# Kernel tuning notes

Hardware: AMD Instinct MI355X
Metric: run time of the kernel (lower is better)

## Reference

```python
import jax, jax.numpy as jnp
import numpy as np

TEMP = 10.0
D_IN, D_HID, D_OUT = 256, 512, 256
B, M = 4, 4096


def _mlp(x, W1, b1, W2, b2):
    # two-layer MLP, ReLU hidden, linear output ('cnt' = continuous)
    h = jax.nn.relu(jnp.einsum('bmd,dh->bmh', x, W1) + b1)
    return jnp.einsum('bmh,ho->bmo', h, W2) + b2


def setup_inputs() -> dict:
    key = jax.random.key(0)
    ks = jax.random.split(key, 9)
    s1 = 1.0 / np.sqrt(D_IN)
    s2 = 1.0 / np.sqrt(D_HID)
    return {
        'x': jax.random.normal(ks[0], (B, M, D_IN), dtype=jnp.float32),
        'Wq1': jax.random.normal(ks[1], (D_IN, D_HID), dtype=jnp.float32) * s1,
        'bq1': jnp.zeros((D_HID,), dtype=jnp.float32),
        'Wq2': jax.random.normal(ks[2], (D_HID, D_OUT), dtype=jnp.float32) * s2,
        'bq2': jnp.zeros((D_OUT,), dtype=jnp.float32),
        'Wk1': jax.random.normal(ks[3], (D_IN, D_HID), dtype=jnp.float32) * s1,
        'bk1': jnp.zeros((D_HID,), dtype=jnp.float32),
        'Wk2': jax.random.normal(ks[4], (D_HID, D_OUT), dtype=jnp.float32) * s2,
        'bk2': jnp.zeros((D_OUT,), dtype=jnp.float32),
    }


def reference(x, Wq1, bq1, Wq2, bq2, Wk1, bk1, Wk2, bk2):
    queries = _mlp(x, Wq1, bq1, Wq2, bq2)   # [B, M, D_OUT]
    keys = _mlp(x, Wk1, bk1, Wk2, bk2)      # [B, M, D_OUT]
    qkt = jnp.einsum('bnd,bmd->bnm', queries, keys)  # [B, M, M]
    row_max = jnp.max(qkt, axis=-1, keepdims=True)   # row-max normalization (not sqrt(d))
    dist = jax.nn.softmax(TEMP * qkt / row_max, axis=-1)
    return dist
```

## Files before the change

### kernel.cpp

```cpp
#include <hip/hip_runtime.h>
#include <hip/hip_bf16.h>

typedef unsigned short u16;
typedef unsigned int u32;
typedef _Float16 f16;
typedef __attribute__((ext_vector_type(4))) float f32x4;
typedef __attribute__((ext_vector_type(8))) short s16x8;
typedef __attribute__((ext_vector_type(8))) _Float16 f16x8;

__device__ __forceinline__ u16 f2bf(float f) {
    union { float f; u32 u; } v; v.f = f;
    u32 r = v.u + 0x7FFFu + ((v.u >> 16) & 1u);
    return (u16)(r >> 16);
}
__device__ __forceinline__ float bf2f(u16 h) {
    union { u32 u; float f; } v; v.u = ((u32)h) << 16;
    return v.f;
}

__device__ __forceinline__ void gll16(const void* g, void* l) {
    __builtin_amdgcn_global_load_lds(
        (const __attribute__((address_space(1))) void*)g,
        (__attribute__((address_space(3))) void*)l, 16, 0, 0);
}


__global__ __launch_bounds__(256) void split_x_kernel(
    const float* __restrict__ x, u16* __restrict__ hi, u16* __restrict__ lo) {
    int i = blockIdx.x * 256 + threadIdx.x;
    float4 v = ((const float4*)x)[i];
    u16 h0 = f2bf(v.x), h1 = f2bf(v.y), h2 = f2bf(v.z), h3 = f2bf(v.w);
    ushort4 h, l;
    h.x = h0; h.y = h1; h.z = h2; h.w = h3;
    l.x = f2bf(v.x - bf2f(h0)); l.y = f2bf(v.y - bf2f(h1));
    l.z = f2bf(v.z - bf2f(h2)); l.w = f2bf(v.w - bf2f(h3));
    ((ushort4*)hi)[i] = h; ((ushort4*)lo)[i] = l;
}

__global__ __launch_bounds__(256) void split_wT_kernel(
    const float* __restrict__ Wq1, const float* __restrict__ Wk1,
    const float* __restrict__ Wq2, const float* __restrict__ Wk2,
    u16* __restrict__ w1hi, u16* __restrict__ w1lo,
    u16* __restrict__ w2hi, u16* __restrict__ w2lo) {
    int y = blockIdx.y;
    const float* src = (y == 0) ? Wq1 : (y == 1) ? Wk1 : (y == 2) ? Wq2 : Wk2;
    int R = (y < 2) ? 256 : 512;
    int C = (y < 2) ? 512 : 256;
    u16* dh = ((y < 2) ? w1hi : w2hi) + (y & 1) * 131072;
    u16* dl = ((y < 2) ? w1lo : w2lo) + (y & 1) * 131072;
    int i = blockIdx.x * 256 + threadIdx.x;
    int c = i / R, r = i - c * R;
    float v = src[(size_t)r * C + c];
    u16 h = f2bf(v);
    dh[i] = h; dl[i] = f2bf(v - bf2f(h));
}

__global__ void pack_bias(const float* __restrict__ bq1, const float* __restrict__ bk1,
                          const float* __restrict__ bq2, const float* __restrict__ bk2,
                          float* __restrict__ b1, float* __restrict__ b2) {
    int t = threadIdx.x;
    b1[t] = bq1[t]; b1[512 + t] = bk1[t];
    if (t < 256) { b2[t] = bq2[t]; b2[256 + t] = bk2[t]; }
}

#define BM 128
#define BN 128
#define BK 64

template<int SPLIT_OUT, int RELU, int SPLITB, int F16S>
__global__ __launch_bounds__(256, 2)
void gemm_bt(const u16* __restrict__ Ahi, const u16* __restrict__ Alo,
             const u16* __restrict__ Bhi, const u16* __restrict__ Blo,
             const float* __restrict__ bias, long biasBatch,
             void* __restrict__ Cout, u16* __restrict__ Chi, u16* __restrict__ Clo,
             int M, int N, int K,
             long aBatch, long bBatch, long cBatch) {
    __shared__ u16 lds[(3 + SPLITB) * BM * BK];
    const int tid = threadIdx.x;
    const int wave = tid >> 6, lane = tid & 63;

    u32 gx = gridDim.x, gy = gridDim.y, gz = gridDim.z;
    u32 flat = (blockIdx.z * gy + blockIdx.y) * gx + blockIdx.x;
    u32 nwg = gx * gy * gz;
    u32 bx, by, bz;
    if ((nwg & 7u) == 0u) {
        u32 cpx = nwg >> 3;
        u32 nf = (flat & 7u) * cpx + (flat >> 3);
        bx = nf % gx; u32 t = nf / gx; by = t % gy; bz = t / gy;
    } else {
        bx = blockIdx.x; by = blockIdx.y; bz = blockIdx.z;
    }

    const long m0 = (long)by * BM, n0 = (long)bx * BN;

    const u16* pAhi = Ahi + (size_t)bz * aBatch;
    const u16* pAlo = Alo + (size_t)bz * aBatch;
    const u16* pBhi = Bhi + (size_t)bz * bBatch;
    const u16* pBlo = Blo + (size_t)bz * bBatch;

    int srow[4], scol[4];
#pragma unroll
    for (int i = 0; i < 4; i++) {
        int lin = wave * 4096 + i * 1024 + lane * 16;
        srow[i] = lin >> 7;
        scol[i] = (lin & 127) >> 1;
    }

    const int wr = wave >> 1, wc = wave & 1;
    const int lrow = lane & 15, kgrp = lane >> 4;

    f32x4 acc[4][4] = {};

    const int ksteps = K / BK;
    for (int kt = 0; kt < ksteps; ++kt) {
#pragma unroll
        for (int i = 0; i < 4; i++) {
            size_t ga = (size_t)(m0 + srow[i]) * K + (size_t)kt * BK + scol[i];
            size_t gb = (size_t)(n0 + srow[i]) * K + (size_t)kt * BK + scol[i];
            u32 lb = (u32)(wave * 4096 + i * 1024);
            gll16(pAhi + ga, (char*)lds + 0 * 16384 + lb);
            gll16(pAlo + ga, (char*)lds + 1 * 16384 + lb);
            gll16(pBhi + gb, (char*)lds + 2 * 16384 + lb);
            if constexpr (SPLITB) gll16(pBlo + gb, (char*)lds + 3 * 16384 + lb);
        }
        __syncthreads();
#pragma unroll
        for (int kk = 0; kk < 2; ++kk) {
            s16x8 ah[4], al[4], bh[4], bl[4];
            const int ko = kk * 32 + kgrp * 8;
#pragma unroll
            for (int m = 0; m < 4; m++) {
                int r = wr * 64 + m * 16 + lrow;
                ah[m] = *(const s16x8*)&lds[0 * 8192 + r * 64 + ko];
                al[m] = *(const s16x8*)&lds[1 * 8192 + r * 64 + ko];
            }
#pragma unroll
            for (int n = 0; n < 4; n++) {
                int r = wc * 64 + n * 16 + lrow;
                bh[n] = *(const s16x8*)&lds[2 * 8192 + r * 64 + ko];
                if constexpr (SPLITB) bl[n] = *(const s16x8*)&lds[3 * 8192 + r * 64 + ko];
            }
#pragma unroll
            for (int m = 0; m < 4; m++)
#pragma unroll
                for (int n = 0; n < 4; n++) {
                    acc[m][n] = __builtin_amdgcn_mfma_f32_16x16x32_bf16(ah[m], bh[n], acc[m][n], 0, 0, 0);
                    if constexpr (SPLITB)
                        acc[m][n] = __builtin_amdgcn_mfma_f32_16x16x32_bf16(ah[m], bl[n], acc[m][n], 0, 0, 0);
                    acc[m][n] = __builtin_amdgcn_mfma_f32_16x16x32_bf16(al[m], bh[n], acc[m][n], 0, 0, 0);
                }
        }
        __syncthreads();
    }

    if constexpr (SPLIT_OUT || F16S) {
        u16* sh  = (u16*)lds;
        u16* slo = (u16*)lds + 16384;
#pragma unroll
        for (int m = 0; m < 4; m++) {
#pragma unroll
            for (int n = 0; n < 4; n++) {
                int col_l = wc * 64 + n * 16 + lrow;
                float bv = 0.f;
                if constexpr (SPLIT_OUT) bv = bias[bz * biasBatch + n0 + col_l];
#pragma unroll
                for (int j = 0; j < 4; j++) {
                    int row_l = wr * 64 + m * 16 + kgrp * 4 + j;
                    int sc = col_l ^ (((row_l >> 2) & 3) << 4);
                    float v = acc[m][n][j];
                    if constexpr (SPLIT_OUT) {
                        v += bv;
                        if (RELU) v = fmaxf(v, 0.f);
                        u16 h = f2bf(v);
                        sh[row_l * 128 + sc]  = h;
                        slo[row_l * 128 + sc] = f2bf(v - bf2f(h));
                    } else {
                        union { f16 f; u16 u; } cv; cv.f = (f16)v;
                        sh[row_l * 128 + sc] = cv.u;
                    }
                }
            }
        }
        __syncthreads();
#pragma unroll
        for (int i = 0; i < 8; i++) {
            int idx = i * 256 + tid;
            int row_l = idx >> 4;
            int c8 = (idx & 15) << 3;
            int sc = c8 ^ (((row_l >> 2) & 3) << 4);
            size_t go = (size_t)bz * cBatch + (size_t)(m0 + row_l) * N + n0 + c8;
            s16x8 vh = *(const s16x8*)&sh[row_l * 128 + sc];
            if constexpr (SPLIT_OUT) {
                s16x8 vl = *(const s16x8*)&slo[row_l * 128 + sc];
                *(s16x8*)&Chi[go] = vh;
                *(s16x8*)&Clo[go] = vl;
            } else {
                *(s16x8*)&((u16*)Cout)[go] = vh;
            }
        }
    } else {
#pragma unroll
        for (int m = 0; m < 4; m++)
#pragma unroll
            for (int n = 0; n < 4; n++) {
                long col = n0 + wc * 64 + n * 16 + lrow;
#pragma unroll
                for (int j = 0; j < 4; j++) {
                    long row = m0 + wr * 64 + m * 16 + kgrp * 4 + j;
                    ((float*)Cout)[(size_t)bz * cBatch + (size_t)row * N + col] = acc[m][n][j];
                }
            }
    }
}

__global__ __launch_bounds__(256) void softmax_rows(float* __restrict__ S) {
    const int tid = threadIdx.x;
    float* p = S + (size_t)blockIdx.x * 4096;
    float4 v[4];
    float lmax = -3.4e38f;
#pragma unroll
    for (int i = 0; i < 4; i++) {
        v[i] = ((float4*)p)[tid + 256 * i];
        lmax = fmaxf(lmax, fmaxf(fmaxf(v[i].x, v[i].y), fmaxf(v[i].z, v[i].w)));
    }
#pragma unroll
    for (int o = 32; o; o >>= 1) lmax = fmaxf(lmax, __shfl_xor(lmax, o));
    __shared__ float redm[4];
    __shared__ float reds[4];
    if ((tid & 63) == 0) redm[tid >> 6] = lmax;
    __syncthreads();
    const float m = fmaxf(fmaxf(redm[0], redm[1]), fmaxf(redm[2], redm[3]));
    const float c = 10.0f / m;
    float s = 0.f;
#pragma unroll
    for (int i = 0; i < 4; i++) {
        v[i].x = expf(c * v[i].x - 10.0f);
        v[i].y = expf(c * v[i].y - 10.0f);
        v[i].z = expf(c * v[i].z - 10.0f);
        v[i].w = expf(c * v[i].w - 10.0f);
        s += v[i].x + v[i].y + v[i].z + v[i].w;
    }
#pragma unroll
    for (int o = 32; o; o >>= 1) s += __shfl_xor(s, o);
    if ((tid & 63) == 0) reds[tid >> 6] = s;
    __syncthreads();
    const float inv = 1.0f / (reds[0] + reds[1] + reds[2] + reds[3]);
#pragma unroll
    for (int i = 0; i < 4; i++) {
        v[i].x *= inv; v[i].y *= inv; v[i].z *= inv; v[i].w *= inv;
        ((float4*)p)[tid + 256 * i] = v[i];
    }
}

__global__ __launch_bounds__(256) void softmax_f16(const f16* __restrict__ S,
                                                   float* __restrict__ O) {
    const int tid = threadIdx.x;
    const f16* p = S + (size_t)blockIdx.x * 4096;
    float* o = O + (size_t)blockIdx.x * 4096;
    f16x8 a0 = ((const f16x8*)p)[tid];
    f16x8 a1 = ((const f16x8*)p)[tid + 256];
    float v[16];
#pragma unroll
    for (int j = 0; j < 8; j++) { v[j] = (float)a0[j]; v[8 + j] = (float)a1[j]; }
    float lmax = -3.4e38f;
#pragma unroll
    for (int j = 0; j < 16; j++) lmax = fmaxf(lmax, v[j]);
#pragma unroll
    for (int off = 32; off; off >>= 1) lmax = fmaxf(lmax, __shfl_xor(lmax, off));
    __shared__ float redm[4];
    __shared__ float reds[4];
    if ((tid & 63) == 0) redm[tid >> 6] = lmax;
    __syncthreads();
    const float m = fmaxf(fmaxf(redm[0], redm[1]), fmaxf(redm[2], redm[3]));
    const float c = 10.0f / m;
    float s = 0.f;
#pragma unroll
    for (int j = 0; j < 16; j++) { v[j] = expf(c * v[j] - 10.0f); s += v[j]; }
#pragma unroll
    for (int off = 32; off; off >>= 1) s += __shfl_xor(s, off);
    if ((tid & 63) == 0) reds[tid >> 6] = s;
    __syncthreads();
    const float inv = 1.0f / (reds[0] + reds[1] + reds[2] + reds[3]);
    float4 w;
#pragma unroll
    for (int q = 0; q < 4; q++) {
        int base = q * 4;
        w.x = v[base + 0] * inv; w.y = v[base + 1] * inv;
        w.z = v[base + 2] * inv; w.w = v[base + 3] * inv;
        int idx = (q < 2) ? (2 * tid + q) : (2 * tid + 512 + (q - 2));
        ((float4*)o)[idx] = w;
    }
}

extern "C" void kernel_launch(void* const* d_in, const int* in_sizes, int n_in,
                              void* d_out, int out_size, void* d_ws, size_t ws_size,
                              hipStream_t stream) {
    const float* x   = (const float*)d_in[0];
    const float* Wq1 = (const float*)d_in[1];
    const float* bq1 = (const float*)d_in[2];
    const float* Wq2 = (const float*)d_in[3];
    const float* bq2 = (const float*)d_in[4];
    const float* Wk1 = (const float*)d_in[5];
    const float* bk1 = (const float*)d_in[6];
    const float* Wk2 = (const float*)d_in[7];
    const float* bk2 = (const float*)d_in[8];
    float* out = (float*)d_out;

    const size_t MB = 1048576;
    char* ws = (char*)d_ws;
    float* b1 = (float*)(ws);
    float* b2 = (float*)(ws + 4096);
    u16* w1hi = (u16*)(ws + 8 * 1024);
    u16* w1lo = (u16*)(ws + 8 * 1024 + 512 * 1024);
    u16* w2hi = (u16*)(ws + 8 * 1024 + 1024 * 1024);
    u16* w2lo = (u16*)(ws + 8 * 1024 + 1536 * 1024);
    u16* qhi  = (u16*)(ws + 4 * MB);
    u16* khi  = (u16*)(ws + 12 * MB);
    u16* qlo  = (u16*)(ws + 20 * MB);
    u16* klo  = (u16*)(ws + 28 * MB);
    f16* S16  = (f16*)(ws + 36 * MB);

    const bool f16s = (ws_size >= 164 * MB);

    char* ob = (char*)d_out;
    u16* xhi = (u16*)(ob + 0 * MB);
    u16* xlo = (u16*)(ob + 8 * MB);
    u16* Hhi = (u16*)(ob + 16 * MB);
    u16* Hlo = (u16*)(ob + 48 * MB);

    split_x_kernel<<<4096, 256, 0, stream>>>(x, xhi, xlo);
    split_wT_kernel<<<dim3(512, 4), 256, 0, stream>>>(Wq1, Wk1, Wq2, Wk2,
                                                      w1hi, w1lo, w2hi, w2lo);
    pack_bias<<<1, 512, 0, stream>>>(bq1, bk1, bq2, bk2, b1, b2);

    gemm_bt<1, 1, 1, 0><<<dim3(4, 128, 2), 256, 0, stream>>>(
        xhi, xlo, w1hi, w1lo, b1, 512,
        nullptr, Hhi, Hlo,
        16384, 512, 256,
        0L, 131072L, 8388608L);

    gemm_bt<1, 0, 1, 0><<<dim3(2, 128, 2), 256, 0, stream>>>(
        Hhi, Hlo, w2hi, w2lo, b2, 256,
        nullptr, qhi, qlo,
        16384, 256, 512,
        8388608L, 131072L, 4194304L);

    if (f16s) {
        gemm_bt<0, 0, 0, 1><<<dim3(32, 32, 4), 256, 0, stream>>>(
            qhi, qlo, khi, klo, nullptr, 0,
            (void*)S16, nullptr, nullptr,
            4096, 4096, 256,
            1048576L, 1048576L, 16777216L);
        softmax_f16<<<16384, 256, 0, stream>>>(S16, out);
    } else {
        gemm_bt<0, 0, 0, 0><<<dim3(32, 32, 4), 256, 0, stream>>>(
            qhi, qlo, khi, klo, nullptr, 0,
            (void*)out, nullptr, nullptr,
            4096, 4096, 256,
            1048576L, 1048576L, 16777216L);
        softmax_rows<<<16384, 256, 0, stream>>>(out);
    }
}
```

Before: 468.7 us.

## Double-buffer GEMM LDS tiles with half-depth K steps to overlap loads

The GEMM main loop now splits the LDS into two buffers of BK=32 tiles instead of one BK=64 tile. It issues the global-to-LDS loads for the next K step before running the MFMA work on the current buffer, so memory latency can hide behind compute. This also drops one barrier per iteration. In exchange each step does half the compute between barriers, and the 64-byte LDS row stride may change bank-conflict behaviour. Total LDS size stays the same.

```diff
diff --git a/kernel.cpp b/kernel.cpp
--- a/kernel.cpp
+++ b/kernel.cpp
@@ -65,7 +65,7 @@
 
 #define BM 128
 #define BN 128
-#define BK 64
+#define BKT 32
 
 template<int SPLIT_OUT, int RELU, int SPLITB, int F16S>
 __global__ __launch_bounds__(256, 2)
@@ -75,7 +75,11 @@
              void* __restrict__ Cout, u16* __restrict__ Chi, u16* __restrict__ Clo,
              int M, int N, int K,
              long aBatch, long bBatch, long cBatch) {
-    __shared__ u16 lds[(3 + SPLITB) * BM * BK];
+    constexpr int NMAT  = 3 + SPLITB;
+    constexpr int TILEU = BM * BKT;
+    constexpr int HALFU = NMAT * TILEU;
+    __shared__ u16 lds[2 * HALFU];
+
     const int tid = threadIdx.x;
     const int wave = tid >> 6, lane = tid & 63;
 
@@ -98,60 +102,71 @@
     const u16* pBhi = Bhi + (size_t)bz * bBatch;
     const u16* pBlo = Blo + (size_t)bz * bBatch;
 
-    int srow[4], scol[4];
-#pragma unroll
-    for (int i = 0; i < 4; i++) {
-        int lin = wave * 4096 + i * 1024 + lane * 16;
-        srow[i] = lin >> 7;
-        scol[i] = (lin & 127) >> 1;
+    int srow[2], scol[2];
+#pragma unroll
+    for (int i = 0; i < 2; i++) {
+        int lin = i * 4096 + tid * 16;
+        srow[i] = lin >> 6;
+        scol[i] = (lin & 63) >> 1;
     }
 
     const int wr = wave >> 1, wc = wave & 1;
     const int lrow = lane & 15, kgrp = lane >> 4;
+    const int ko = kgrp * 8;
 
     f32x4 acc[4][4] = {};
 
-    const int ksteps = K / BK;
-    for (int kt = 0; kt < ksteps; ++kt) {
-#pragma unroll
-        for (int i = 0; i < 4; i++) {
-            size_t ga = (size_t)(m0 + srow[i]) * K + (size_t)kt * BK + scol[i];
-            size_t gb = (size_t)(n0 + srow[i]) * K + (size_t)kt * BK + scol[i];
-            u32 lb = (u32)(wave * 4096 + i * 1024);
-            gll16(pAhi + ga, (char*)lds + 0 * 16384 + lb);
-            gll16(pAlo + ga, (char*)lds + 1 * 16384 + lb);
-            gll16(pBhi + gb, (char*)lds + 2 * 16384 + lb);
-            if constexpr (SPLITB) gll16(pBlo + gb, (char*)lds + 3 * 16384 + lb);
-        }
+    auto stage = [&](int b, int kt) {
+#pragma unroll
+        for (int i = 0; i < 2; i++) {
+            size_t ga = (size_t)(m0 + srow[i]) * K + (size_t)kt * BKT + scol[i];
+            size_t gb = (size_t)(n0 + srow[i]) * K + (size_t)kt * BKT + scol[i];
+            u32 lb = (u32)(b * (HALFU * 2) + i * 4096 + wave * 1024);
+            gll16(pAhi + ga, (char*)lds + 0 * 8192 + lb);
+            gll16(pAlo + ga, (char*)lds + 1 * 8192 + lb);
+            gll16(pBhi + gb, (char*)lds + 2 * 8192 + lb);
+            if constexpr (SPLITB) gll16(pBlo + gb, (char*)lds + 3 * 8192 + lb);
+        }
+    };
+
+    auto compute = [&](int b) {
+        const u16* B0 = lds + b * HALFU;
+        s16x8 ah[4], al[4], bh[4], bl[4];
+#pragma unroll
+        for (int m = 0; m < 4; m++) {
+            int r = wr * 64 + m * 16 + lrow;
+            ah[m] = *(const s16x8*)&B0[0 * TILEU + r * 32 + ko];
+            al[m] = *(const s16x8*)&B0[1 * TILEU + r * 32 + ko];
+        }
+#pragma unroll
+        for (int n = 0; n < 4; n++) {
+            int r = wc * 64 + n * 16 + lrow;
+            bh[n] = *(const s16x8*)&B0[2 * TILEU + r * 32 + ko];
+            if constexpr (SPLITB) bl[n] = *(const s16x8*)&B0[3 * TILEU + r * 32 + ko];
+        }
+#pragma unroll
+        for (int m = 0; m < 4; m++)
+#pragma unroll
+            for (int n = 0; n < 4; n++) {
+                acc[m][n] = __builtin_amdgcn_mfma_f32_16x16x32_bf16(ah[m], bh[n], acc[m][n], 0, 0, 0);
+                if constexpr (SPLITB)
+                    acc[m][n] = __builtin_amdgcn_mfma_f32_16x16x32_bf16(ah[m], bl[n], acc[m][n], 0, 0, 0);
+                acc[m][n] = __builtin_amdgcn_mfma_f32_16x16x32_bf16(al[m], bh[n], acc[m][n], 0, 0, 0);
+            }
+    };
+
+    const int ksteps = K / BKT;
+    stage(0, 0);
+    __syncthreads();
+    int cur = 0;
+    for (int kt = 0; kt < ksteps - 1; ++kt) {
+        stage(cur ^ 1, kt + 1);
+        compute(cur);
         __syncthreads();
-#pragma unroll
-        for (int kk = 0; kk < 2; ++kk) {
-            s16x8 ah[4], al[4], bh[4], bl[4];
-            const int ko = kk * 32 + kgrp * 8;
-#pragma unroll
-            for (int m = 0; m < 4; m++) {
-                int r = wr * 64 + m * 16 + lrow;
-                ah[m] = *(const s16x8*)&lds[0 * 8192 + r * 64 + ko];
-                al[m] = *(const s16x8*)&lds[1 * 8192 + r * 64 + ko];
-            }
-#pragma unroll
-            for (int n = 0; n < 4; n++) {
-                int r = wc * 64 + n * 16 + lrow;
-                bh[n] = *(const s16x8*)&lds[2 * 8192 + r * 64 + ko];
-                if constexpr (SPLITB) bl[n] = *(const s16x8*)&lds[3 * 8192 + r * 64 + ko];
-            }
-#pragma unroll
-            for (int m = 0; m < 4; m++)
-#pragma unroll
-                for (int n = 0; n < 4; n++) {
-                    acc[m][n] = __builtin_amdgcn_mfma_f32_16x16x32_bf16(ah[m], bh[n], acc[m][n], 0, 0, 0);
-                    if constexpr (SPLITB)
-                        acc[m][n] = __builtin_amdgcn_mfma_f32_16x16x32_bf16(ah[m], bl[n], acc[m][n], 0, 0, 0);
-                    acc[m][n] = __builtin_amdgcn_mfma_f32_16x16x32_bf16(al[m], bh[n], acc[m][n], 0, 0, 0);
-                }
-        }
-        __syncthreads();
-    }
+        cur ^= 1;
+    }
+    compute(cur);
+    __syncthreads();
 
     if constexpr (SPLIT_OUT || F16S) {
         u16* sh  = (u16*)lds;
```

New measurement: 460.5 us. No clear change (-1.8%).
